# Kernel tuning notes

Hardware: AMD Instinct MI355X
Metric: run time of the kernel (lower is better)

Reference implementation:

```python
import jax, jax.numpy as jnp
import numpy as np

B, T, E, V, NH = 2, 2048, 2048, 4096, 8
KD = E // NH   # key_dim = 256
HD = V // NH   # head_dim = 512
EPS = 1e-6


def _rotate_every_two(x):
    x1 = x[..., ::2]
    x2 = x[..., 1::2]
    return jnp.stack((-x2, x1), axis=-1).reshape(x.shape)


def _theta_shift(x, sin, cos):
    return x * cos + _rotate_every_two(x) * sin


def setup_inputs() -> dict:
    key = jax.random.key(0)
    ks = jax.random.split(key, 6)
    hidden_states = jax.random.normal(ks[0], (B, T, E), dtype=jnp.float32)
    g = 2.0 ** -2.5  # xavier-ish gain
    Wq = jax.random.normal(ks[1], (E, E), dtype=jnp.float32) * (g / np.sqrt(E))
    Wk = jax.random.normal(ks[2], (E, E), dtype=jnp.float32) * (g / np.sqrt(E))
    Wv = jax.random.normal(ks[3], (V, E), dtype=jnp.float32) * (g / np.sqrt(E))
    Wg = jax.random.normal(ks[4], (V, E), dtype=jnp.float32) * (g / np.sqrt(E))
    Wo = jax.random.normal(ks[5], (E, V), dtype=jnp.float32) * (g / np.sqrt(V))
    # RetNet rotary-like angles: [T, key_dim]
    angle = 1.0 / (10000.0 ** jnp.linspace(0.0, 1.0, KD // 2))
    angle = jnp.repeat(angle, 2)                          # [KD]
    index = jnp.arange(T, dtype=jnp.float32)
    sin = jnp.sin(index[:, None] * angle[None, :])        # [T, KD]
    cos = jnp.cos(index[:, None] * angle[None, :])
    # per-head decay mask: gamma_h^(i-j) for i>=j, row-normalized by sqrt(sum)
    gamma = 1.0 - 2.0 ** (-5.0 - jnp.arange(NH, dtype=jnp.float32))  # [NH]
    idx = jnp.arange(T)
    diff = idx[:, None] - idx[None, :]                    # [T, T]
    valid = diff >= 0
    dm = jnp.where(valid, gamma[:, None, None] ** jnp.maximum(diff, 0)[None], 0.0)  # [NH,T,T]
    dm = dm / jnp.sqrt(dm.sum(-1, keepdims=True))
    decay_mask = jnp.nan_to_num(dm)[None]                 # [1, NH, T, T]
    return {"hidden_states": hidden_states, "sin": sin, "cos": cos,
            "decay_mask": decay_mask, "Wq": Wq, "Wk": Wk, "Wv": Wv,
            "Wg": Wg, "Wo": Wo}


def reference(hidden_states, sin, cos, decay_mask, Wq, Wk, Wv, Wg, Wo):
    b, t, e = hidden_states.shape
    nh = decay_mask.shape[1]
    kd = e // nh
    x = hidden_states
    q = (x @ Wq.T).reshape(b, t, nh, kd).transpose(0, 2, 1, 3)   # [B,NH,T,KD]
    k = (x @ Wk.T).reshape(b, t, nh, kd).transpose(0, 2, 1, 3)
    v = (x @ Wv.T)
    hd = v.shape[-1] // nh
    v = v.reshape(b, t, nh, hd).transpose(0, 2, 1, 3)            # [B,NH,T,HD]
    g = x @ Wg.T                                                 # [B,T,V]
    k = k * (kd ** -0.5)
    qr = _theta_shift(q, sin, cos)
    kr = _theta_shift(k, sin, cos)
    # parallel retention
    retention = jnp.einsum('bhik,bhjk->bhij', qr, kr) * decay_mask
    denom = jnp.clip(jnp.abs(jax.lax.stop_gradient(retention)).sum(-1, keepdims=True), 1.0, 5e4)
    retention = retention / denom
    out = jnp.einsum('bhij,bhjd->bhid', retention, v)            # [B,NH,T,HD]
    out = out.transpose(0, 2, 1, 3)                              # [B,T,NH,HD]
    # RMSNorm over head_dim, no affine, in fp32
    of = out.astype(jnp.float32)
    normed = (of * jax.lax.rsqrt(jnp.mean(of * of, axis=-1, keepdims=True) + EPS)).astype(out.dtype)
    normed = normed.reshape(b, t, nh * hd)                       # [B,T,V]
    gated = jax.nn.swish(g) * normed
    return gated @ Wo.T                                          # [B,T,E]
```

## Files before the change

### kernel.cpp

```cpp
#include <hip/hip_runtime.h>
#include <hip/hip_bf16.h>

typedef _Float16 half8 __attribute__((ext_vector_type(8)));
typedef float f32x4 __attribute__((ext_vector_type(4)));

__device__ __forceinline__ unsigned short f2h(float f) {
  _Float16 h = (_Float16)f;
  return __builtin_bit_cast(unsigned short, h);
}
__device__ __forceinline__ float h2f(unsigned short u) {
  return (float)__builtin_bit_cast(_Float16, u);
}

__device__ __forceinline__ void gload16(const unsigned short* g, unsigned short* l) {
  __builtin_amdgcn_global_load_lds(
      (const __attribute__((address_space(1))) unsigned int*)g,
      (__attribute__((address_space(3))) unsigned int*)l, 16, 0, 0);
}

__global__ __launch_bounds__(256) void cvt_f32_f16_kernel(
    const float* __restrict__ in, unsigned short* __restrict__ out, int n4) {
  int i = blockIdx.x * 256 + threadIdx.x;
  if (i < n4) {
    float4 v = ((const float4*)in)[i];
    ushort4 o;
    o.x = f2h(v.x); o.y = f2h(v.y); o.z = f2h(v.z); o.w = f2h(v.w);
    ((ushort4*)out)[i] = o;
  }
}

template <int EPI>
__global__ __launch_bounds__(256) void gemm_nt(
    const unsigned short* __restrict__ A, const unsigned short* __restrict__ Bm,
    unsigned short* __restrict__ Ch, unsigned short* __restrict__ Ch2,
    float* __restrict__ Cf, int M, int N, int K,
    const float* __restrict__ sintab, const float* __restrict__ costab) {
  __shared__ __align__(16) unsigned short As[128 * 64];
  __shared__ __align__(16) unsigned short Bs[128 * 64];
  const int tid = threadIdx.x;
  const int lane = tid & 63, w = tid >> 6;
  const int wm = w >> 1, wn = w & 1;
  const int m0 = blockIdx.y * 128, n0 = blockIdx.x * 128;
  const int lrow = lane & 15, lk = lane >> 4;
  const int sw = (lane & 7) << 4;

  f32x4 acc[4][4] = {};
  const int KT = K >> 6;
  for (int kt = 0; kt < KT; ++kt) {
    __syncthreads();
#pragma unroll
    for (int q = 0; q < 4; ++q) {
      int base16 = q * 256 + w * 64;
      int idx16 = base16 + lane;
      int row = idx16 >> 3;
      int qb = (idx16 & 7) * 16;
      int qbs = qb ^ ((row & 7) << 4);
      gload16(A + ((size_t)(m0 + row) * K + kt * 64 + (qbs >> 1)), &As[base16 * 8]);
      gload16(Bm + ((size_t)(n0 + row) * K + kt * 64 + (qbs >> 1)), &Bs[base16 * 8]);
    }
    __syncthreads();
#pragma unroll
    for (int k2 = 0; k2 < 2; ++k2) {
      half8 af[4], bf[4];
      int kb = k2 * 64 + lk * 16;
#pragma unroll
      for (int i = 0; i < 4; ++i) {
        int ra = wm * 64 + i * 16 + lrow;
        af[i] = *(const half8*)((const char*)As + ra * 128 + (kb ^ sw));
        int rb = wn * 64 + i * 16 + lrow;
        bf[i] = *(const half8*)((const char*)Bs + rb * 128 + (kb ^ sw));
      }
#pragma unroll
      for (int i = 0; i < 4; ++i)
#pragma unroll
        for (int j = 0; j < 4; ++j)
          acc[i][j] = __builtin_amdgcn_mfma_f32_16x16x32_f16(af[i], bf[j], acc[i][j], 0, 0, 0);
    }
  }
#pragma unroll
  for (int i = 0; i < 4; ++i) {
#pragma unroll
    for (int j = 0; j < 4; ++j) {
      int col = wn * 64 + j * 16 + lrow;
      int gn = n0 + col;
#pragma unroll
      for (int r = 0; r < 4; ++r) {
        int gm = m0 + wm * 64 + i * 16 + lk * 4 + r;
        float v = acc[i][j][r];
        if (EPI == 1) {
          float p = __shfl_xor(v, 1);
          int t = gm & 2047, d = gn & 255;
          float c = costab[t * 256 + d], s = sintab[t * 256 + d];
          float rot = (lane & 1) ? p : -p;
          float o = v * c + rot * s;
          if (gn < 2048) Ch[(size_t)gm * 2048 + gn] = f2h(o);
          else Ch2[(size_t)gm * 2048 + (gn - 2048)] = f2h(0.0625f * o);
        } else if (EPI == 2) {
          if (gn < 4096) Ch[(size_t)gm * 4096 + gn] = f2h(v);
          else Ch2[(size_t)gm * 4096 + (gn - 4096)] = f2h(v / (1.0f + expf(-v)));
        } else if (EPI == 3) {
          Cf[(size_t)gm * N + gn] = v;
        } else {
          Ch[(size_t)gm * N + gn] = f2h(v);
        }
      }
    }
  }
}

__global__ __launch_bounds__(256) void transpose_v_kernel(
    const unsigned short* __restrict__ vv, unsigned short* __restrict__ vT) {
  __shared__ __align__(16) unsigned short tile[64][72];
  int t0 = blockIdx.x * 64;
  int n0 = blockIdx.y * 64;
  int b = blockIdx.z;
  int tid = threadIdx.x;
#pragma unroll
  for (int q = 0; q < 2; ++q) {
    int idx = q * 256 + tid;
    int r = idx >> 3, c8 = (idx & 7) * 8;
    const unsigned short* src = vv + ((size_t)(b * 2048 + t0 + r)) * 4096 + n0 + c8;
    *(uint4*)&tile[r][c8] = *(const uint4*)src;
  }
  __syncthreads();
#pragma unroll
  for (int q = 0; q < 2; ++q) {
    int idx = q * 256 + tid;
    int rn = idx >> 3, c8 = (idx & 7) * 8;
    unsigned short tmp[8];
#pragma unroll
    for (int e = 0; e < 8; ++e) tmp[e] = tile[c8 + e][rn];
    unsigned short* dst = vT + ((size_t)b * 4096 + n0 + rn) * 2048 + t0 + c8;
    *(uint4*)dst = *(uint4*)tmp;
  }
}

__global__ __launch_bounds__(256, 2) void retention_kernel(
    const unsigned short* __restrict__ qr, const unsigned short* __restrict__ kr,
    const unsigned short* __restrict__ vT, const unsigned short* __restrict__ sg,
    unsigned short* __restrict__ gated) {
  __shared__ __align__(16) unsigned short Ks[64 * 256];
  __shared__ __align__(16) unsigned short Vs[256 * 64];
  __shared__ __align__(16) unsigned short Ss[64 * 64];
  const int T = 2048, E = 2048, Vd = 4096;
  const int tid = threadIdx.x, lane = tid & 63, w = tid >> 6;
  const int lrow = lane & 15, lk = lane >> 4, sw = (lane & 7) << 4;
  const int ib = blockIdx.x, h = blockIdx.y, b = blockIdx.z;
  const int i0 = ib * 64;

  const float omg = exp2f(-5.0f - (float)h);
  const float l2g = log2f(1.0f - omg);
  float rni[4];
#pragma unroll
  for (int r = 0; r < 4; ++r) {
    int gi = i0 + w * 16 + lk * 4 + r;
    rni[r] = rsqrtf((1.0f - exp2f((float)(gi + 1) * l2g)) / omg);
  }

  half8 qf[8];
  {
    const unsigned short* qrow =
        qr + ((size_t)(b * T + i0 + w * 16 + lrow)) * E + h * 256 + lk * 8;
#pragma unroll
    for (int kt = 0; kt < 8; ++kt) qf[kt] = *(const half8*)(qrow + kt * 32);
  }
  f32x4 accv[32] = {};
  float rowAbs[4] = {0.f, 0.f, 0.f, 0.f};

  const unsigned short* krB = kr + ((size_t)(b * T)) * E + h * 256;
  const unsigned short* vtB = vT + ((size_t)b * Vd + h * 512) * T;

  for (int jt = 0; jt <= ib; ++jt) {
    int j0 = jt * 64;
    __syncthreads();
#pragma unroll
    for (int q = 0; q < 8; ++q) {
      int base16 = q * 256 + w * 64;
      int idx16 = base16 + lane;
      int row = idx16 >> 5;
      int qb = (idx16 & 31) * 16;
      int qbs = qb ^ ((row & 7) << 4);
      gload16(krB + (size_t)(j0 + row) * E + (qbs >> 1), &Ks[base16 * 8]);
    }
#pragma unroll
    for (int q = 0; q < 8; ++q) {
      int base16 = q * 256 + w * 64;
      int idx16 = base16 + lane;
      int row = idx16 >> 3;
      int qb = (idx16 & 7) * 16;
      int qbs = qb ^ ((row & 7) << 4);
      gload16(vtB + (size_t)row * T + j0 + (qbs >> 1), &Vs[base16 * 8]);
    }
    __syncthreads();

    f32x4 sacc[4] = {};
#pragma unroll
    for (int kt = 0; kt < 8; ++kt) {
      int kb = kt * 64 + lk * 16;
#pragma unroll
      for (int c = 0; c < 4; ++c) {
        int row = c * 16 + lrow;
        half8 kf = *(const half8*)((const char*)Ks + row * 512 + (kb ^ sw));
        sacc[c] = __builtin_amdgcn_mfma_f32_16x16x32_f16(qf[kt], kf, sacc[c], 0, 0, 0);
      }
    }
#pragma unroll
    for (int c = 0; c < 4; ++c) {
#pragma unroll
      for (int r = 0; r < 4; ++r) {
        int rl = lk * 4 + r;
        int gi = i0 + w * 16 + rl;
        int gj = j0 + c * 16 + lrow;
        int diff = gi - gj;
        float dmv = (diff >= 0) ? exp2f((float)diff * l2g) * rni[r] : 0.0f;
        float sv = sacc[c][r] * dmv;
        rowAbs[r] += fabsf(sv);
        int srow = w * 16 + rl;
        int scb = (c * 16 + lrow) * 2;
        *(unsigned short*)((char*)Ss + srow * 128 + (scb ^ ((srow & 7) << 4))) = f2h(sv);
      }
    }
    half8 sfr[2];
#pragma unroll
    for (int k2 = 0; k2 < 2; ++k2) {
      int rowS = w * 16 + lrow;
      sfr[k2] = *(const half8*)((const char*)Ss + rowS * 128 + ((k2 * 64 + lk * 16) ^ sw));
    }
#pragma unroll
    for (int nc = 0; nc < 16; ++nc) {
#pragma unroll
      for (int k2 = 0; k2 < 2; ++k2) {
        int rowV = nc * 16 + lrow;
        half8 vf = *(const half8*)((const char*)Vs + rowV * 128 + ((k2 * 64 + lk * 16) ^ sw));
        accv[nc] = __builtin_amdgcn_mfma_f32_16x16x32_f16(sfr[k2], vf, accv[nc], 0, 0, 0);
      }
    }
    __syncthreads();
#pragma unroll
    for (int q = 0; q < 8; ++q) {
      int base16 = q * 256 + w * 64;
      int idx16 = base16 + lane;
      int row = idx16 >> 3;
      int qb = (idx16 & 7) * 16;
      int qbs = qb ^ ((row & 7) << 4);
      gload16(vtB + (size_t)(256 + row) * T + j0 + (qbs >> 1), &Vs[base16 * 8]);
    }
    __syncthreads();
#pragma unroll
    for (int nc = 0; nc < 16; ++nc) {
#pragma unroll
      for (int k2 = 0; k2 < 2; ++k2) {
        int rowV = nc * 16 + lrow;
        half8 vf = *(const half8*)((const char*)Vs + rowV * 128 + ((k2 * 64 + lk * 16) ^ sw));
        accv[16 + nc] = __builtin_amdgcn_mfma_f32_16x16x32_f16(sfr[k2], vf, accv[16 + nc], 0, 0, 0);
      }
    }
  }

#pragma unroll
  for (int r = 0; r < 4; ++r) {
    float v = rowAbs[r];
    v += __shfl_xor(v, 1); v += __shfl_xor(v, 2);
    v += __shfl_xor(v, 4); v += __shfl_xor(v, 8);
    rowAbs[r] = fminf(fmaxf(v, 1.0f), 50000.0f);
  }
  float ssum[4] = {0.f, 0.f, 0.f, 0.f};
#pragma unroll
  for (int nc = 0; nc < 32; ++nc)
#pragma unroll
    for (int r = 0; r < 4; ++r) {
      float v = accv[nc][r] / rowAbs[r];
      accv[nc][r] = v;
      ssum[r] += v * v;
    }
#pragma unroll
  for (int r = 0; r < 4; ++r) {
    float v = ssum[r];
    v += __shfl_xor(v, 1); v += __shfl_xor(v, 2);
    v += __shfl_xor(v, 4); v += __shfl_xor(v, 8);
    ssum[r] = rsqrtf(v * (1.0f / 512.0f) + 1e-6f);
  }
#pragma unroll
  for (int r = 0; r < 4; ++r) {
    int gi = i0 + w * 16 + lk * 4 + r;
    size_t rowoff = ((size_t)(b * T + gi)) * Vd + h * 512;
#pragma unroll
    for (int nc = 0; nc < 32; ++nc) {
      int col = nc * 16 + lrow;
      float gv = h2f(sg[rowoff + col]);
      gated[rowoff + col] = f2h(accv[nc][r] * ssum[r] * gv);
    }
  }
}

extern "C" void kernel_launch(void* const* d_in, const int* in_sizes, int n_in,
                              void* d_out, int out_size, void* d_ws, size_t ws_size,
                              hipStream_t stream) {
  (void)in_sizes; (void)n_in; (void)out_size; (void)ws_size;
  const float* hidden = (const float*)d_in[0];
  const float* sintab = (const float*)d_in[1];
  const float* costab = (const float*)d_in[2];
  const float* Wq = (const float*)d_in[4];
  const float* Wk = (const float*)d_in[5];
  const float* Wv = (const float*)d_in[6];
  const float* Wg = (const float*)d_in[7];
  const float* Wo = (const float*)d_in[8];
  float* outp = (float*)d_out;
  char* ws = (char*)d_ws;
  const size_t MiB = (size_t)1 << 20;
  unsigned short* xb    = (unsigned short*)(ws + 0 * MiB);
  unsigned short* WqkH  = (unsigned short*)(ws + 16 * MiB);
  unsigned short* WvgH  = (unsigned short*)(ws + 32 * MiB);
  unsigned short* WoH   = (unsigned short*)(ws + 64 * MiB);
  unsigned short* qrb   = (unsigned short*)(ws + 80 * MiB);
  unsigned short* krb   = (unsigned short*)(ws + 96 * MiB);
  unsigned short* vvb   = (unsigned short*)(ws + 112 * MiB);
  unsigned short* vTb   = (unsigned short*)(ws + 144 * MiB);
  unsigned short* sgb   = (unsigned short*)(ws + 176 * MiB);
  unsigned short* gatedb = vvb;

  auto cvt = [&](const float* in, unsigned short* out, int n) {
    cvt_f32_f16_kernel<<<dim3((n / 4 + 255) / 256), 256, 0, stream>>>(in, out, n / 4);
  };
  cvt(hidden, xb, 4096 * 2048);
  cvt(Wq, WqkH, 2048 * 2048);
  cvt(Wk, WqkH + 2048 * 2048, 2048 * 2048);
  cvt(Wv, WvgH, 4096 * 2048);
  cvt(Wg, WvgH + 4096 * 2048, 4096 * 2048);
  cvt(Wo, WoH, 2048 * 4096);

  gemm_nt<1><<<dim3(32, 32), 256, 0, stream>>>(xb, WqkH, qrb, krb, nullptr,
                                               4096, 4096, 2048, sintab, costab);
  gemm_nt<2><<<dim3(64, 32), 256, 0, stream>>>(xb, WvgH, vvb, sgb, nullptr,
                                               4096, 8192, 2048, nullptr, nullptr);
  transpose_v_kernel<<<dim3(32, 64, 2), 256, 0, stream>>>(vvb, vTb);
  retention_kernel<<<dim3(32, 8, 2), 256, 0, stream>>>(qrb, krb, vTb, sgb, gatedb);
  gemm_nt<3><<<dim3(16, 32), 256, 0, stream>>>(gatedb, WoH, nullptr, nullptr, outp,
                                               4096, 2048, 4096, nullptr, nullptr);
}
```

Before: 1.150 ms.

## Repartition retention S·V across waves, load full V tile, reverse block order, swizzle GEMM grid

```diff
diff --git a/kernel.cpp b/kernel.cpp
--- a/kernel.cpp
+++ b/kernel.cpp
@@ -40,7 +40,12 @@
   const int tid = threadIdx.x;
   const int lane = tid & 63, w = tid >> 6;
   const int wm = w >> 1, wn = w & 1;
-  const int m0 = blockIdx.y * 128, n0 = blockIdx.x * 128;
+  const int gx = gridDim.x;
+  const int nwg = gx * gridDim.y;
+  const int wgid = blockIdx.y * gx + blockIdx.x;
+  const int q8 = nwg >> 3;
+  const int swz = (wgid & 7) * q8 + (wgid >> 3);
+  const int m0 = (swz / gx) * 128, n0 = (swz % gx) * 128;
   const int lrow = lane & 15, lk = lane >> 4;
   const int sw = (lane & 7) << 4;
 
@@ -135,17 +140,20 @@
   }
 }
 
-__global__ __launch_bounds__(256, 2) void retention_kernel(
+__global__ __launch_bounds__(256, 1) void retention_kernel(
     const unsigned short* __restrict__ qr, const unsigned short* __restrict__ kr,
     const unsigned short* __restrict__ vT, const unsigned short* __restrict__ sg,
     unsigned short* __restrict__ gated) {
   __shared__ __align__(16) unsigned short Ks[64 * 256];
-  __shared__ __align__(16) unsigned short Vs[256 * 64];
+  __shared__ __align__(16) unsigned short Vs[512 * 64];
   __shared__ __align__(16) unsigned short Ss[64 * 64];
+  __shared__ float denomL[64];
+  __shared__ float ssumL[64][4];
   const int T = 2048, E = 2048, Vd = 4096;
   const int tid = threadIdx.x, lane = tid & 63, w = tid >> 6;
   const int lrow = lane & 15, lk = lane >> 4, sw = (lane & 7) << 4;
-  const int ib = blockIdx.x, h = blockIdx.y, b = blockIdx.z;
+  const int ib = 31 - blockIdx.x;
+  const int h = blockIdx.y, b = blockIdx.z;
   const int i0 = ib * 64;
 
   const float omg = exp2f(-5.0f - (float)h);
@@ -164,7 +172,7 @@
 #pragma unroll
     for (int kt = 0; kt < 8; ++kt) qf[kt] = *(const half8*)(qrow + kt * 32);
   }
-  f32x4 accv[32] = {};
+  f32x4 accv[4][8] = {};
   float rowAbs[4] = {0.f, 0.f, 0.f, 0.f};
 
   const unsigned short* krB = kr + ((size_t)(b * T)) * E + h * 256;
@@ -183,7 +191,7 @@
       gload16(krB + (size_t)(j0 + row) * E + (qbs >> 1), &Ks[base16 * 8]);
     }
 #pragma unroll
-    for (int q = 0; q < 8; ++q) {
+    for (int q = 0; q < 16; ++q) {
       int base16 = q * 256 + w * 64;
       int idx16 = base16 + lane;
       int row = idx16 >> 3;
@@ -220,39 +228,25 @@
         *(unsigned short*)((char*)Ss + srow * 128 + (scb ^ ((srow & 7) << 4))) = f2h(sv);
       }
     }
-    half8 sfr[2];
-#pragma unroll
-    for (int k2 = 0; k2 < 2; ++k2) {
-      int rowS = w * 16 + lrow;
-      sfr[k2] = *(const half8*)((const char*)Ss + rowS * 128 + ((k2 * 64 + lk * 16) ^ sw));
-    }
-#pragma unroll
-    for (int nc = 0; nc < 16; ++nc) {
+    __syncthreads();
+
+    half8 sfr[4][2];
+#pragma unroll
+    for (int s = 0; s < 4; ++s)
 #pragma unroll
       for (int k2 = 0; k2 < 2; ++k2) {
-        int rowV = nc * 16 + lrow;
+        int rowS = s * 16 + lrow;
+        sfr[s][k2] = *(const half8*)((const char*)Ss + rowS * 128 + ((k2 * 64 + lk * 16) ^ sw));
+      }
+#pragma unroll
+    for (int dt = 0; dt < 8; ++dt) {
+#pragma unroll
+      for (int k2 = 0; k2 < 2; ++k2) {
+        int rowV = w * 128 + dt * 16 + lrow;
         half8 vf = *(const half8*)((const char*)Vs + rowV * 128 + ((k2 * 64 + lk * 16) ^ sw));
-        accv[nc] = __builtin_amdgcn_mfma_f32_16x16x32_f16(sfr[k2], vf, accv[nc], 0, 0, 0);
-      }
-    }
-    __syncthreads();
-#pragma unroll
-    for (int q = 0; q < 8; ++q) {
-      int base16 = q * 256 + w * 64;
-      int idx16 = base16 + lane;
-      int row = idx16 >> 3;
-      int qb = (idx16 & 7) * 16;
-      int qbs = qb ^ ((row & 7) << 4);
-      gload16(vtB + (size_t)(256 + row) * T + j0 + (qbs >> 1), &Vs[base16 * 8]);
-    }
-    __syncthreads();
-#pragma unroll
-    for (int nc = 0; nc < 16; ++nc) {
-#pragma unroll
-      for (int k2 = 0; k2 < 2; ++k2) {
-        int rowV = nc * 16 + lrow;
-        half8 vf = *(const half8*)((const char*)Vs + rowV * 128 + ((k2 * 64 + lk * 16) ^ sw));
-        accv[16 + nc] = __builtin_amdgcn_mfma_f32_16x16x32_f16(sfr[k2], vf, accv[16 + nc], 0, 0, 0);
+#pragma unroll
+        for (int s = 0; s < 4; ++s)
+          accv[s][dt] = __builtin_amdgcn_mfma_f32_16x16x32_f16(sfr[s][k2], vf, accv[s][dt], 0, 0, 0);
       }
     }
   }
@@ -262,33 +256,43 @@
     float v = rowAbs[r];
     v += __shfl_xor(v, 1); v += __shfl_xor(v, 2);
     v += __shfl_xor(v, 4); v += __shfl_xor(v, 8);
-    rowAbs[r] = fminf(fmaxf(v, 1.0f), 50000.0f);
-  }
-  float ssum[4] = {0.f, 0.f, 0.f, 0.f};
-#pragma unroll
-  for (int nc = 0; nc < 32; ++nc)
+    v = fminf(fmaxf(v, 1.0f), 50000.0f);
+    if (lrow == 0) denomL[w * 16 + lk * 4 + r] = v;
+  }
+  __syncthreads();
+#pragma unroll
+  for (int s = 0; s < 4; ++s) {
 #pragma unroll
     for (int r = 0; r < 4; ++r) {
-      float v = accv[nc][r] / rowAbs[r];
-      accv[nc][r] = v;
-      ssum[r] += v * v;
-    }
-#pragma unroll
-  for (int r = 0; r < 4; ++r) {
-    float v = ssum[r];
-    v += __shfl_xor(v, 1); v += __shfl_xor(v, 2);
-    v += __shfl_xor(v, 4); v += __shfl_xor(v, 8);
-    ssum[r] = rsqrtf(v * (1.0f / 512.0f) + 1e-6f);
-  }
-#pragma unroll
-  for (int r = 0; r < 4; ++r) {
-    int gi = i0 + w * 16 + lk * 4 + r;
-    size_t rowoff = ((size_t)(b * T + gi)) * Vd + h * 512;
-#pragma unroll
-    for (int nc = 0; nc < 32; ++nc) {
-      int col = nc * 16 + lrow;
-      float gv = h2f(sg[rowoff + col]);
-      gated[rowoff + col] = f2h(accv[nc][r] * ssum[r] * gv);
+      float den = denomL[s * 16 + lk * 4 + r];
+      float ss = 0.f;
+#pragma unroll
+      for (int dt = 0; dt < 8; ++dt) {
+        float v = accv[s][dt][r] / den;
+        accv[s][dt][r] = v;
+        ss += v * v;
+      }
+      ss += __shfl_xor(ss, 1); ss += __shfl_xor(ss, 2);
+      ss += __shfl_xor(ss, 4); ss += __shfl_xor(ss, 8);
+      if (lrow == 0) ssumL[s * 16 + lk * 4 + r][w] = ss;
+    }
+  }
+  __syncthreads();
+#pragma unroll
+  for (int s = 0; s < 4; ++s) {
+#pragma unroll
+    for (int r = 0; r < 4; ++r) {
+      int row = s * 16 + lk * 4 + r;
+      float tot = ssumL[row][0] + ssumL[row][1] + ssumL[row][2] + ssumL[row][3];
+      float rstd = rsqrtf(tot * (1.0f / 512.0f) + 1e-6f);
+      int gi = i0 + row;
+      size_t rowoff = ((size_t)(b * T + gi)) * Vd + h * 512 + w * 128;
+#pragma unroll
+      for (int dt = 0; dt < 8; ++dt) {
+        int col = dt * 16 + lrow;
+        float gv = h2f(sg[rowoff + col]);
+        gated[rowoff + col] = f2h(accv[s][dt][r] * rstd * gv);
+      }
     }
   }
 }
```

Result: faster. 936.6 us (-18.6%).
